# Performance work log

Hardware: AMD Instinct MI355X
Metric: run time of the kernel (lower is better)

Reference implementation:

```python
import jax, jax.numpy as jnp
import numpy as np
import math

B, C, H, W = 16, 512, 32, 32
GROUPS = 32
EPS = 1e-5


def group_norm(x, w, b):
    # x: [B, C, H, W]; normalize within each of GROUPS channel groups over (C//G, H, W)
    Bx, Cx, Hx, Wx = x.shape
    xg = x.reshape(Bx, GROUPS, Cx // GROUPS, Hx, Wx)
    mean = xg.mean(axis=(2, 3, 4), keepdims=True)
    var = xg.var(axis=(2, 3, 4), keepdims=True)
    xg = (xg - mean) * jax.lax.rsqrt(var + EPS)
    xn = xg.reshape(Bx, Cx, Hx, Wx)
    return xn * w[None, :, None, None] + b[None, :, None, None]


def setup_inputs() -> dict:
    key = jax.random.key(0)
    ks = jax.random.split(key, 4)
    x = jax.random.normal(ks[0], (B, C, H, W), dtype=jnp.float32)
    gn_w = jnp.ones((C,), dtype=jnp.float32)
    gn_b = jnp.zeros((C,), dtype=jnp.float32)
    # Conv2d 1x1 weights as [out, in] matrices; PyTorch default init scale
    qkv_w = jax.random.normal(ks[1], (3 * C, C), dtype=jnp.float32) * (1.0 / math.sqrt(C))
    qkv_b = jnp.zeros((3 * C,), dtype=jnp.float32)
    out_w = jax.random.normal(ks[2], (C, C), dtype=jnp.float32) * (1.0 / math.sqrt(C))
    out_b = jnp.zeros((C,), dtype=jnp.float32)
    return {"x": x, "gn_w": gn_w, "gn_b": gn_b, "qkv_w": qkv_w,
            "qkv_b": qkv_b, "out_w": out_w, "out_b": out_b}


def reference(x, gn_w, gn_b, qkv_w, qkv_b, out_w, out_b):
    Bx, Cx, Hx, Wx = x.shape
    N = Hx * Wx
    h = group_norm(x, gn_w, gn_b)                       # [B, C, H, W]
    hf = h.reshape(Bx, Cx, N)                           # [B, C, N]
    # 1x1 conv == channel matmul
    qkv = jnp.einsum('oc,bcn->bon', qkv_w, hf) + qkv_b[None, :, None]  # [B, 3C, N]
    q, k, v = jnp.split(qkv, 3, axis=1)                 # each [B, C, N]
    q = q.transpose(0, 2, 1)                            # [B, N, C]
    v = v.transpose(0, 2, 1)                            # [B, N, C]
    scale = 1.0 / math.sqrt(Cx)
    attn = jnp.einsum('bnc,bcm->bnm', q, k) * scale     # [B, N, N]
    attn = jax.nn.softmax(attn, axis=-1)
    o = jnp.einsum('bnm,bmc->bnc', attn, v)             # [B, N, C]
    o = o.transpose(0, 2, 1)                            # [B, C, N]
    o = jnp.einsum('oc,bcn->bon', out_w, o) + out_b[None, :, None]
    return x + o.reshape(Bx, Cx, Hx, Wx)
```

## Files before the change

### kernel.cpp

```cpp
#include <hip/hip_runtime.h>

typedef unsigned short u16;
typedef short short8 __attribute__((ext_vector_type(8)));
typedef float floatx4 __attribute__((ext_vector_type(4)));
typedef u16 u16x4 __attribute__((ext_vector_type(4)));
typedef u16 u16x8 __attribute__((ext_vector_type(8)));

#define DEVI __device__ __forceinline__

#define LDH 544
#define LDQ 1088
#define LDV 16448

DEVI u16 f2bf(float x) {
    union { float f; unsigned u; } c; c.f = x;
    unsigned u = c.u;
    u += 0x7fffu + ((u >> 16) & 1u);
    return (u16)(u >> 16);
}
DEVI float bf2f(u16 h) {
    union { unsigned u; float f; } c; c.u = ((unsigned)h) << 16;
    return c.f;
}

DEVI void gload_lds16(const void* g, void* l) {
    auto gp = (const __attribute__((address_space(1))) unsigned*)(unsigned long long)g;
    auto lp = (__attribute__((address_space(3))) unsigned*)(unsigned)(unsigned long long)l;
    __builtin_amdgcn_global_load_lds(gp, lp, 16, 0, 0);
}

__global__ __launch_bounds__(256) void prepgn_kernel(const float* __restrict__ x,
                                                     const float* __restrict__ gw,
                                                     const float* __restrict__ gb,
                                                     u16* __restrict__ h,
                                                     const float* __restrict__ qkv_w, u16* __restrict__ wqb,
                                                     const float* __restrict__ out_w, u16* __restrict__ wob,
                                                     u16* __restrict__ wvT,
                                                     const float* __restrict__ qkv_b, float* __restrict__ dv) {
    const int bid = blockIdx.x;
    const int t = threadIdx.x;
    if (bid < 512) {
        const int b = bid >> 5, g = bid & 31;
        const float* xg = x + (long long)bid * 16384;
        const int n0 = t * 4;

        float4 xv[16];
        float s = 0.f, s2 = 0.f;
        #pragma unroll
        for (int cc = 0; cc < 16; cc++) {
            xv[cc] = *(const float4*)&xg[cc * 1024 + n0];
            s  += xv[cc].x + xv[cc].y + xv[cc].z + xv[cc].w;
            s2 += xv[cc].x*xv[cc].x + xv[cc].y*xv[cc].y + xv[cc].z*xv[cc].z + xv[cc].w*xv[cc].w;
        }
        #pragma unroll
        for (int m = 1; m < 64; m <<= 1) { s += __shfl_xor(s, m, 64); s2 += __shfl_xor(s2, m, 64); }
        __shared__ float rs[4], rq[4];
        if ((t & 63) == 0) { rs[t >> 6] = s; rq[t >> 6] = s2; }
        __syncthreads();
        float mean = (rs[0] + rs[1] + rs[2] + rs[3]) * (1.f / 16384.f);
        float var  = (rq[0] + rq[1] + rq[2] + rq[3]) * (1.f / 16384.f) - mean * mean;
        float rstd = rsqrtf(var + 1e-5f);

        u16x8 o[4][2];
        #pragma unroll
        for (int cc = 0; cc < 16; cc++) {
            int c = g * 16 + cc;
            float sc = gw[c] * rstd;
            float sh = gb[c] - mean * sc;
            o[0][cc >> 3][cc & 7] = f2bf(xv[cc].x * sc + sh);
            o[1][cc >> 3][cc & 7] = f2bf(xv[cc].y * sc + sh);
            o[2][cc >> 3][cc & 7] = f2bf(xv[cc].z * sc + sh);
            o[3][cc >> 3][cc & 7] = f2bf(xv[cc].w * sc + sh);
        }
        u16* hb = h + ((long long)b * 1024 + n0) * LDH + g * 16;
        #pragma unroll
        for (int k = 0; k < 4; k++) {
            *(u16x8*)&hb[(long long)k * LDH]     = o[k][0];
            *(u16x8*)&hb[(long long)k * LDH + 8] = o[k][1];
        }
    } else if (bid < 1280) {
        int i = (bid - 512) * 256 + t;
        const float* src; u16* dst; int j;
        if (i < 131072) { src = qkv_w; dst = wqb; j = i; }
        else            { src = out_w; dst = wob; j = i - 131072; }
        float4 v = *(const float4*)&src[j * 4];
        u16x4 p; p[0] = f2bf(v.x); p[1] = f2bf(v.y); p[2] = f2bf(v.z); p[3] = f2bf(v.w);
        *(u16x4*)&dst[j * 4] = p;
    } else if (bid < 1296) {
        __shared__ u16 tile[128][132];
        const int tb = bid - 1280;
        const int vbase = (tb >> 2) * 128, cbase = (tb & 3) * 128;
        #pragma unroll
        for (int rnd = 0; rnd < 16; rnd++) {
            int row = rnd * 8 + (t >> 5);
            int c4  = (t & 31) * 4;
            float4 v = *(const float4*)&qkv_w[(long long)(1024 + vbase + row) * 512 + cbase + c4];
            tile[row][c4 + 0] = f2bf(v.x);
            tile[row][c4 + 1] = f2bf(v.y);
            tile[row][c4 + 2] = f2bf(v.z);
            tile[row][c4 + 3] = f2bf(v.w);
        }
        __syncthreads();
        #pragma unroll
        for (int rnd = 0; rnd < 8; rnd++) {
            int r  = rnd * 16 + (t >> 4);
            int ch = (t & 15) * 8;
            u16x8 o;
            #pragma unroll
            for (int e = 0; e < 8; e++) o[e] = tile[ch + e][r];
            *(u16x8*)&wvT[(long long)(cbase + r) * 512 + vbase + ch] = o;
        }
    } else {
        int o = (bid - 1296) * 256 + t;
        const float4* r = (const float4*)(out_w + (long long)o * 512);
        const float4* b = (const float4*)(qkv_b + 1024);
        float s = 0.f;
        #pragma unroll 4
        for (int c = 0; c < 128; c++) {
            float4 a = r[c], q = b[c];
            s += a.x*q.x + a.y*q.y + a.z*q.z + a.w*q.w;
        }
        dv[o] = s;
    }
}

__global__ __launch_bounds__(256) void lreduce_kernel(const float* __restrict__ ps,
                                                      float* __restrict__ invl) {
    int i = blockIdx.x * 256 + threadIdx.x;
    int z = i >> 10, n = i & 1023;
    float l = 0.f;
    #pragma unroll
    for (int kb = 0; kb < 8; kb++) l += ps[((z * 8 + kb) << 10) + n];
    invl[i] = 1.f / l;
}

template <int MODE, bool STATS, bool FOLDW>
__global__ __launch_bounds__(256, 3)
void gemm_bt_kernel(const u16* __restrict__ A, const u16* __restrict__ Bt,
                    void* __restrict__ C0,
                    const float* __restrict__ bias, const float* __restrict__ res,
                    float* __restrict__ aux,
                    const u16* __restrict__ A2, const u16* __restrict__ B2, u16* __restrict__ C2,
                    float scale, int lda, int ldb, int ldc,
                    long long sA, long long sB, long long sC, long long sR, int K) {
    int bx = blockIdx.x, by = blockIdx.y;
    const int bz = blockIdx.z;
    bool isW = false;
    int ldA = lda, ldB = ldb, ldC = ldc;
    const u16* Ap = A;
    const u16* Bp = Bt;
    if (FOLDW && bx >= 128) {
        isW = true;
        const int tb = (bx - 128) * 8 + by;
        bx = tb & 3; by = tb >> 2;
        Ap = A2; Bp = B2;
        ldA = 512; ldB = 512; ldC = 512;
    }
    const int t    = threadIdx.x;
    const int lane = t & 63;
    const int wave = t >> 6;
    const int m0   = by * 128;
    const int n0   = bx * 128;
    Ap += (long long)bz * sA;
    Bp += (long long)bz * sB;

    __shared__ __align__(16) u16 smem[16384];
    u16* As = smem;
    u16* Bs = smem + 8192;

    const int wm = wave >> 1, wn = wave & 1;
    const int quad = lane >> 4, lrow = lane & 15;

    floatx4 acc[4][4];
    #pragma unroll
    for (int i = 0; i < 4; i++)
        #pragma unroll
        for (int j = 0; j < 4; j++)
            #pragma unroll
            for (int r = 0; r < 4; r++) acc[i][j][r] = 0.f;

    const int rowA = t >> 2;
    const int kch  = (t & 3) * 8;
    const u16* Ag = Ap + (long long)(m0 + rowA) * ldA + kch;
    const u16* Bg = Bp + (long long)(n0 + rowA) * ldB + kch;
    u16* Al = &As[t * 8];
    u16* Bl = &Bs[t * 8];
    const long long a64 = (long long)64 * ldA;
    const long long b64 = (long long)64 * ldB;

    for (int k0 = 0; k0 < K; k0 += 64) {
        gload_lds16(Ag + k0,            Al);
        gload_lds16(Ag + k0 + a64,      Al + 2048);
        gload_lds16(Ag + k0 + 32,       Al + 4096);
        gload_lds16(Ag + k0 + 32 + a64, Al + 6144);
        gload_lds16(Bg + k0,            Bl);
        gload_lds16(Bg + k0 + b64,      Bl + 2048);
        gload_lds16(Bg + k0 + 32,       Bl + 4096);
        gload_lds16(Bg + k0 + 32 + b64, Bl + 6144);
        __syncthreads();
        #pragma unroll
        for (int kk = 0; kk < 2; kk++) {
            short8 af[4], bfr[4];
            #pragma unroll
            for (int i = 0; i < 4; i++)
                af[i] = *(const short8*)&As[kk*4096 + (wm*64 + i*16 + lrow)*32 + quad*8];
            #pragma unroll
            for (int j = 0; j < 4; j++)
                bfr[j] = *(const short8*)&Bs[kk*4096 + (wn*64 + j*16 + lrow)*32 + quad*8];
            #pragma unroll
            for (int i = 0; i < 4; i++)
                #pragma unroll
                for (int j = 0; j < 4; j++)
                    acc[i][j] = __builtin_amdgcn_mfma_f32_16x16x32_bf16(af[i], bfr[j], acc[i][j], 0, 0, 0);
        }
        __syncthreads();
    }

    const int ST = 136;

    if (MODE == 1 || isW) {
        u16* Cbase = isW ? C2 : (u16*)C0;
        #pragma unroll
        for (int p = 0; p < 4; p++) {
            if (p) __syncthreads();
            if (wm == (p >> 1)) {
                #pragma unroll
                for (int ii = 0; ii < 2; ii++) {
                    const int i = (p & 1) * 2 + ii;
                    const int row = ii * 16 + quad * 4;
                    #pragma unroll
                    for (int j = 0; j < 4; j++) {
                        const int cB = wn * 64 + j * 16 + lrow;
                        #pragma unroll
                        for (int r = 0; r < 4; r++) {
                            float v = acc[i][j][r] * scale;
                            if (STATS) v = __expf(v);
                            else if (!isW && bias) v += bias[m0 + p * 32 + row + r];
                            smem[(row + r) * ST + cB] = f2bf(v);
                        }
                    }
                }
            }
            __syncthreads();
            const int rr = t >> 3, cc = (t & 7) * 16;
            u16x8 a0 = *(u16x8*)&smem[rr * ST + cc];
            u16x8 a1 = *(u16x8*)&smem[rr * ST + cc + 8];
            u16* Cp = Cbase + (long long)bz * sC + (long long)(m0 + p * 32 + rr) * ldC + n0 + cc;
            *(u16x8*)Cp = a0;
            *(u16x8*)(Cp + 8) = a1;
            if (STATS) {
                float ls = 0.f;
                #pragma unroll
                for (int e = 0; e < 8; e++)
                    ls += bf2f(a0[e]) + bf2f(a1[e]);
                #pragma unroll
                for (int m2 = 1; m2 < 8; m2 <<= 1) ls += __shfl_xor(ls, m2, 8);
                if ((t & 7) == 0)
                    aux[((long long)(bz * 8 + bx)) * 1024 + m0 + p * 32 + rr] = ls;
            }
        }
    } else if (MODE == 2) {
        #pragma unroll
        for (int p = 0; p < 4; p++) {
            if (p) __syncthreads();
            if (wn == (p >> 1)) {
                #pragma unroll
                for (int jj = 0; jj < 2; jj++) {
                    const int j = (p & 1) * 2 + jj;
                    const int row = jj * 16 + lrow;
                    #pragma unroll
                    for (int i = 0; i < 4; i++) {
                        const int mmL = wm * 64 + i * 16 + quad * 4;
                        u16x4 pk;
                        #pragma unroll
                        for (int r = 0; r < 4; r++)
                            pk[r] = f2bf(acc[i][j][r] + bias[m0 + mmL + r]);
                        *(u16x4*)&smem[row * ST + mmL] = pk;
                    }
                }
            }
            __syncthreads();
            const int rr = t >> 3, cc = (t & 7) * 16;
            u16x8 a0 = *(u16x8*)&smem[rr * ST + cc];
            u16x8 a1 = *(u16x8*)&smem[rr * ST + cc + 8];
            u16* Cp = (u16*)C0 + (long long)(n0 + p * 32 + rr) * ldC + m0 + cc;
            *(u16x8*)Cp = a0;
            *(u16x8*)(Cp + 8) = a1;
        }
    } else {
        float* smf = (float*)smem;
        const int SF = 132;
        float* C = (float*)C0 + (long long)bz * sC;
        const float* rz = res + (long long)bz * sR;
        const float* il = aux + (long long)bz * 1024;
        #pragma unroll
        for (int p = 0; p < 8; p++) {
            if (p) __syncthreads();
            if (wm == (p >> 2)) {
                const int i = p & 3;
                #pragma unroll
                for (int j = 0; j < 4; j++) {
                    const int cB = wn * 64 + j * 16 + lrow;
                    #pragma unroll
                    for (int r = 0; r < 4; r++)
                        smf[(quad * 4 + r) * SF + cB] = acc[i][j][r];
                }
            }
            __syncthreads();
            const int rr = t >> 4, cc = (t & 15) * 8;
            const float bsv = bias[m0 + p * 16 + rr];
            float4 il0 = *(const float4*)&il[n0 + cc];
            float4 il1 = *(const float4*)&il[n0 + cc + 4];
            const long long gro = (long long)(m0 + p * 16 + rr) * ldC + n0 + cc;
            float4 rv0 = *(const float4*)&rz[gro];
            float4 rv1 = *(const float4*)&rz[gro + 4];
            float4 ov0, ov1;
            ov0.x = smf[rr*SF + cc + 0] * il0.x + bsv + rv0.x;
            ov0.y = smf[rr*SF + cc + 1] * il0.y + bsv + rv0.y;
            ov0.z = smf[rr*SF + cc + 2] * il0.z + bsv + rv0.z;
            ov0.w = smf[rr*SF + cc + 3] * il0.w + bsv + rv0.w;
            ov1.x = smf[rr*SF + cc + 4] * il1.x + bsv + rv1.x;
            ov1.y = smf[rr*SF + cc + 5] * il1.y + bsv + rv1.y;
            ov1.z = smf[rr*SF + cc + 6] * il1.z + bsv + rv1.z;
            ov1.w = smf[rr*SF + cc + 7] * il1.w + bsv + rv1.w;
            *(float4*)&C[gro]     = ov0;
            *(float4*)&C[gro + 4] = ov1;
        }
    }
}

extern "C" void kernel_launch(void* const* d_in, const int* in_sizes, int n_in,
                              void* d_out, int out_size, void* d_ws, size_t ws_size,
                              hipStream_t stream) {
    (void)in_sizes; (void)n_in; (void)out_size; (void)ws_size;
    const float* x     = (const float*)d_in[0];
    const float* gn_w  = (const float*)d_in[1];
    const float* gn_b  = (const float*)d_in[2];
    const float* qkv_w = (const float*)d_in[3];
    const float* qkv_b = (const float*)d_in[4];
    const float* out_w = (const float*)d_in[5];
    const float* out_b = (const float*)d_in[6];
    float* out = (float*)d_out;

    char* ws = (char*)d_ws;
    u16*  h_t   = (u16*)ws;  ws += (size_t)16*1024*LDH*2;
    u16*  qkv_t = (u16*)ws;  ws += (size_t)16*1024*LDQ*2;
    u16*  vprm  = (u16*)ws;  ws += (size_t)512*LDV*2;
    u16*  E     = (u16*)ws;  ws += (size_t)16*1024*LDQ*2;
    u16*  wqb   = (u16*)ws;  ws += (size_t)1024*512*2;
    u16*  wob   = (u16*)ws;  ws += (size_t)512*512*2;
    u16*  wvT   = (u16*)ws;  ws += (size_t)512*512*2;
    u16*  wprm  = (u16*)ws;  ws += (size_t)512*512*2;
    float* dv   = (float*)ws; ws += (size_t)512*4;
    float* psum = (float*)ws; ws += (size_t)16*8*1024*4;
    float* invl = (float*)ws; ws += (size_t)16*1024*4;

    prepgn_kernel<<<1298, 256, 0, stream>>>(x, gn_w, gn_b, h_t,
                                            qkv_w, wqb, out_w, wob, wvT, qkv_b, dv);

    gemm_bt_kernel<2, false, true><<<dim3(130, 8, 1), 256, 0, stream>>>(
        wqb, h_t, qkv_t, qkv_b, nullptr, nullptr,
        wob, wvT, wprm, 1.0f,
        512, LDH, LDQ, 0, 0, 0, 0, 512);

    gemm_bt_kernel<1, false, false><<<dim3(128, 4, 1), 256, 0, stream>>>(
        wprm, h_t, vprm, dv, nullptr, nullptr,
        nullptr, nullptr, nullptr, 1.0f,
        512, LDH, LDV, 0, 0, 0, 0, 512);

    gemm_bt_kernel<1, true, false><<<dim3(8, 8, 16), 256, 0, stream>>>(
        qkv_t, qkv_t + 512, E, nullptr, nullptr, psum,
        nullptr, nullptr, nullptr, 0.044194173824159216f,
        LDQ, LDQ, LDQ,
        (long long)1024*LDQ, (long long)1024*LDQ, (long long)1024*LDQ, 0, 512);

    lreduce_kernel<<<64, 256, 0, stream>>>(psum, invl);

    gemm_bt_kernel<3, false, false><<<dim3(8, 4, 16), 256, 0, stream>>>(
        vprm, E, out, out_b, x, invl,
        nullptr, nullptr, nullptr, 1.0f,
        LDV, LDQ, 1024,
        1024, (long long)1024*LDQ, (long long)512*1024, (long long)512*1024, 1024);
}
```

Measured before the change: 247.7 us.

## Remap GEMM blocks per XCD, fold row-sum reduction into output GEMM, unpad buffers

The score and output GEMMs now use a 1D grid whose block index is remapped so that all tiles of one batch land on the same XCD, aiming for better L2 reuse of that batch's operands. The separate lreduce kernel is removed: the final GEMM sums the partial softmax denominators itself and keeps the reciprocals in shared memory, saving one launch. Padded leading dimensions (544/1088/16448) are replaced by unpadded strides, which may bring back cache-set or channel conflicts. The score GEMM's launch bound rises to 4 waves per SIMD, and the prep kernel reorders its block roles so the weight conversion runs first.

```diff
diff --git a/kernel.cpp b/kernel.cpp
--- a/kernel.cpp
+++ b/kernel.cpp
@@ -8,10 +8,6 @@
 
 #define DEVI __device__ __forceinline__
 
-#define LDH 544
-#define LDQ 1088
-#define LDV 16448
-
 DEVI u16 f2bf(float x) {
     union { float f; unsigned u; } c; c.f = x;
     unsigned u = c.u;
@@ -29,19 +25,29 @@
     __builtin_amdgcn_global_load_lds(gp, lp, 16, 0, 0);
 }
 
-__global__ __launch_bounds__(256) void prepgn_kernel(const float* __restrict__ x,
-                                                     const float* __restrict__ gw,
-                                                     const float* __restrict__ gb,
-                                                     u16* __restrict__ h,
-                                                     const float* __restrict__ qkv_w, u16* __restrict__ wqb,
-                                                     const float* __restrict__ out_w, u16* __restrict__ wob,
-                                                     u16* __restrict__ wvT,
-                                                     const float* __restrict__ qkv_b, float* __restrict__ dv) {
+__global__ __launch_bounds__(256) void prep_kernel(const float* __restrict__ qkv_w, u16* __restrict__ wq,
+                                                   const float* __restrict__ out_w, u16* __restrict__ wob,
+                                                   u16* __restrict__ wvT,
+                                                   const float* __restrict__ qkv_b, float* __restrict__ dv,
+                                                   const float* __restrict__ x,
+                                                   const float* __restrict__ gw,
+                                                   const float* __restrict__ gb,
+                                                   u16* __restrict__ h) {
     const int bid = blockIdx.x;
     const int t = threadIdx.x;
-    if (bid < 512) {
-        const int b = bid >> 5, g = bid & 31;
-        const float* xg = x + (long long)bid * 16384;
+    __shared__ u16 tile[128][132];
+    if (bid < 768) {
+        int i = bid * 256 + t;
+        const float* src; u16* dst; int j;
+        if (i < 131072) { src = qkv_w; dst = wq; j = i; }
+        else            { src = out_w; dst = wob; j = i - 131072; }
+        float4 v = *(const float4*)&src[j * 4];
+        u16x4 p; p[0] = f2bf(v.x); p[1] = f2bf(v.y); p[2] = f2bf(v.z); p[3] = f2bf(v.w);
+        *(u16x4*)&dst[j * 4] = p;
+    } else if (bid < 1280) {
+        const int bg = bid - 768;
+        const int b = bg >> 5, g = bg & 31;
+        const float* xg = x + (long long)bg * 16384;
         const int n0 = t * 4;
 
         float4 xv[16];
@@ -72,22 +78,13 @@
             o[2][cc >> 3][cc & 7] = f2bf(xv[cc].z * sc + sh);
             o[3][cc >> 3][cc & 7] = f2bf(xv[cc].w * sc + sh);
         }
-        u16* hb = h + ((long long)b * 1024 + n0) * LDH + g * 16;
+        u16* hb = h + ((long long)b * 1024 + n0) * 512 + g * 16;
         #pragma unroll
         for (int k = 0; k < 4; k++) {
-            *(u16x8*)&hb[(long long)k * LDH]     = o[k][0];
-            *(u16x8*)&hb[(long long)k * LDH + 8] = o[k][1];
-        }
-    } else if (bid < 1280) {
-        int i = (bid - 512) * 256 + t;
-        const float* src; u16* dst; int j;
-        if (i < 131072) { src = qkv_w; dst = wqb; j = i; }
-        else            { src = out_w; dst = wob; j = i - 131072; }
-        float4 v = *(const float4*)&src[j * 4];
-        u16x4 p; p[0] = f2bf(v.x); p[1] = f2bf(v.y); p[2] = f2bf(v.z); p[3] = f2bf(v.w);
-        *(u16x4*)&dst[j * 4] = p;
+            *(u16x8*)&hb[(long long)k * 512]     = o[k][0];
+            *(u16x8*)&hb[(long long)k * 512 + 8] = o[k][1];
+        }
     } else if (bid < 1296) {
-        __shared__ u16 tile[128][132];
         const int tb = bid - 1280;
         const int vbase = (tb >> 2) * 128, cbase = (tb & 3) * 128;
         #pragma unroll
@@ -124,18 +121,8 @@
     }
 }
 
-__global__ __launch_bounds__(256) void lreduce_kernel(const float* __restrict__ ps,
-                                                      float* __restrict__ invl) {
-    int i = blockIdx.x * 256 + threadIdx.x;
-    int z = i >> 10, n = i & 1023;
-    float l = 0.f;
-    #pragma unroll
-    for (int kb = 0; kb < 8; kb++) l += ps[((z * 8 + kb) << 10) + n];
-    invl[i] = 1.f / l;
-}
-
-template <int MODE, bool STATS, bool FOLDW>
-__global__ __launch_bounds__(256, 3)
+template <int MODE, int NX, int NY, bool STATS, int MINW = 3, bool FOLDW = false>
+__global__ __launch_bounds__(256, MINW)
 void gemm_bt_kernel(const u16* __restrict__ A, const u16* __restrict__ Bt,
                     void* __restrict__ C0,
                     const float* __restrict__ bias, const float* __restrict__ res,
@@ -143,8 +130,20 @@
                     const u16* __restrict__ A2, const u16* __restrict__ B2, u16* __restrict__ C2,
                     float scale, int lda, int ldb, int ldc,
                     long long sA, long long sB, long long sC, long long sR, int K) {
-    int bx = blockIdx.x, by = blockIdx.y;
-    const int bz = blockIdx.z;
+    int bx, by, bz;
+    if (NX > 0) {
+        const int lid  = blockIdx.x;
+        const int xcd  = lid & 7;
+        const int slot = lid >> 3;
+        const int per  = NX * NY;
+        const int j    = slot / per;
+        const int w    = slot - j * per;
+        bz = xcd + 8 * j;
+        bx = w % NX;
+        by = w / NX;
+    } else {
+        bx = blockIdx.x; by = blockIdx.y; bz = blockIdx.z;
+    }
     bool isW = false;
     int ldA = lda, ldB = ldb, ldC = ldc;
     const u16* Ap = A;
@@ -234,7 +233,7 @@
                         #pragma unroll
                         for (int r = 0; r < 4; r++) {
                             float v = acc[i][j][r] * scale;
-                            if (STATS) v = __expf(v);
+                            if (STATS && !isW) v = __expf(v);
                             else if (!isW && bias) v += bias[m0 + p * 32 + row + r];
                             smem[(row + r) * ST + cB] = f2bf(v);
                         }
@@ -248,7 +247,7 @@
             u16* Cp = Cbase + (long long)bz * sC + (long long)(m0 + p * 32 + rr) * ldC + n0 + cc;
             *(u16x8*)Cp = a0;
             *(u16x8*)(Cp + 8) = a1;
-            if (STATS) {
+            if (STATS && !isW) {
                 float ls = 0.f;
                 #pragma unroll
                 for (int e = 0; e < 8; e++)
@@ -288,11 +287,18 @@
             *(u16x8*)(Cp + 8) = a1;
         }
     } else {
+        __shared__ float sinv[128];
+        if (t < 128) {
+            const float* pz = aux + ((long long)bz * 8) * 1024 + n0 + t;
+            float l = 0.f;
+            #pragma unroll
+            for (int kb = 0; kb < 8; kb++) l += pz[(long long)kb * 1024];
+            sinv[t] = 1.f / l;
+        }
         float* smf = (float*)smem;
         const int SF = 132;
         float* C = (float*)C0 + (long long)bz * sC;
         const float* rz = res + (long long)bz * sR;
-        const float* il = aux + (long long)bz * 1024;
         #pragma unroll
         for (int p = 0; p < 8; p++) {
             if (p) __syncthreads();
@@ -309,8 +315,8 @@
             __syncthreads();
             const int rr = t >> 4, cc = (t & 15) * 8;
             const float bsv = bias[m0 + p * 16 + rr];
-            float4 il0 = *(const float4*)&il[n0 + cc];
-            float4 il1 = *(const float4*)&il[n0 + cc + 4];
+            float4 il0 = *(const float4*)&sinv[cc];
+            float4 il1 = *(const float4*)&sinv[cc + 4];
             const long long gro = (long long)(m0 + p * 16 + rr) * ldC + n0 + cc;
             float4 rv0 = *(const float4*)&rz[gro];
             float4 rv1 = *(const float4*)&rz[gro + 4];
@@ -343,42 +349,39 @@
     float* out = (float*)d_out;
 
     char* ws = (char*)d_ws;
-    u16*  h_t   = (u16*)ws;  ws += (size_t)16*1024*LDH*2;
-    u16*  qkv_t = (u16*)ws;  ws += (size_t)16*1024*LDQ*2;
-    u16*  vprm  = (u16*)ws;  ws += (size_t)512*LDV*2;
-    u16*  E     = (u16*)ws;  ws += (size_t)16*1024*LDQ*2;
-    u16*  wqb   = (u16*)ws;  ws += (size_t)1024*512*2;
+    u16*  h_t   = (u16*)ws;  ws += (size_t)16*1024*512*2;
+    u16*  qkv_t = (u16*)ws;  ws += (size_t)16*1024*1536*2;
+    u16*  vprm  = (u16*)ws;  ws += (size_t)512*16384*2;
+    u16*  E     = (u16*)ws;  ws += (size_t)16*1024*1024*2;
+    u16*  wq    = (u16*)ws;  ws += (size_t)1024*512*2;
     u16*  wob   = (u16*)ws;  ws += (size_t)512*512*2;
     u16*  wvT   = (u16*)ws;  ws += (size_t)512*512*2;
     u16*  wprm  = (u16*)ws;  ws += (size_t)512*512*2;
     float* dv   = (float*)ws; ws += (size_t)512*4;
     float* psum = (float*)ws; ws += (size_t)16*8*1024*4;
-    float* invl = (float*)ws; ws += (size_t)16*1024*4;
-
-    prepgn_kernel<<<1298, 256, 0, stream>>>(x, gn_w, gn_b, h_t,
-                                            qkv_w, wqb, out_w, wob, wvT, qkv_b, dv);
-
-    gemm_bt_kernel<2, false, true><<<dim3(130, 8, 1), 256, 0, stream>>>(
-        wqb, h_t, qkv_t, qkv_b, nullptr, nullptr,
+
+    prep_kernel<<<1298, 256, 0, stream>>>(qkv_w, wq, out_w, wob, wvT, qkv_b, dv,
+                                          x, gn_w, gn_b, h_t);
+
+    gemm_bt_kernel<2, 0, 0, false, 3, true><<<dim3(130, 8, 1), 256, 0, stream>>>(
+        wq, h_t, qkv_t, qkv_b, nullptr, nullptr,
         wob, wvT, wprm, 1.0f,
-        512, LDH, LDQ, 0, 0, 0, 0, 512);
-
-    gemm_bt_kernel<1, false, false><<<dim3(128, 4, 1), 256, 0, stream>>>(
+        512, 512, 1536, 0, 0, 0, 0, 512);
+
+    gemm_bt_kernel<1, 0, 0, false, 3><<<dim3(128, 4, 1), 256, 0, stream>>>(
         wprm, h_t, vprm, dv, nullptr, nullptr,
         nullptr, nullptr, nullptr, 1.0f,
-        512, LDH, LDV, 0, 0, 0, 0, 512);
-
-    gemm_bt_kernel<1, true, false><<<dim3(8, 8, 16), 256, 0, stream>>>(
+        512, 512, 16384, 0, 0, 0, 0, 512);
+
+    gemm_bt_kernel<1, 8, 8, true, 4><<<1024, 256, 0, stream>>>(
         qkv_t, qkv_t + 512, E, nullptr, nullptr, psum,
         nullptr, nullptr, nullptr, 0.044194173824159216f,
-        LDQ, LDQ, LDQ,
-        (long long)1024*LDQ, (long long)1024*LDQ, (long long)1024*LDQ, 0, 512);
-
-    lreduce_kernel<<<64, 256, 0, stream>>>(psum, invl);
-
-    gemm_bt_kernel<3, false, false><<<dim3(8, 4, 16), 256, 0, stream>>>(
-        vprm, E, out, out_b, x, invl,
+        1536, 1536, 1024,
+        (long long)1024*1536, (long long)1024*1536, (long long)1024*1024, 0, 512);
+
+    gemm_bt_kernel<3, 8, 4, false, 3><<<512, 256, 0, stream>>>(
+        vprm, E, out, out_b, x, psum,
         nullptr, nullptr, nullptr, 1.0f,
-        LDV, LDQ, 1024,
-        1024, (long long)1024*LDQ, (long long)512*1024, (long long)512*1024, 1024);
-}
+        16384, 1024, 1024,
+        1024, (long long)1024*1024, (long long)512*1024, (long long)512*1024, 1024);
+}
```

Result: faster. 225.2 us (-9.1%).
